# Performance work log

Measured on AMD Instinct MI355X. Metric: run time of the kernel, lower is better.

## Reference

```python
import jax, jax.numpy as jnp
import numpy as np

N_NODES = 100000
HEADS = 4
HEAD_DIM = 32  # hidden_channels // heads
NEG_SLOPE = 0.2


def gat_layer(x, W, a_src, a_dst, b, src, dst):
    # x: [N, Fin], W: [Fin, H*C], a_src/a_dst: [H, C], b: [H*C]
    N = x.shape[0]
    h = (x @ W).reshape(N, HEADS, HEAD_DIM)            # [N, H, C]
    alpha_s = jnp.einsum('nhc,hc->nh', h, a_src)       # [N, H]
    alpha_d = jnp.einsum('nhc,hc->nh', h, a_dst)       # [N, H]
    e = jax.nn.leaky_relu(alpha_s[src] + alpha_d[dst], NEG_SLOPE)  # [E, H]
    # segment softmax over edges grouped by destination node
    e_max = jax.ops.segment_max(e, dst, num_segments=N)           # [N, H]
    ex = jnp.exp(e - e_max[dst])                                   # [E, H]
    denom = jax.ops.segment_sum(ex, dst, num_segments=N)          # [N, H]
    alpha = ex / denom[dst]                                        # [E, H]
    msg = h[src] * alpha[:, :, None]                               # [E, H, C]
    out = jax.ops.segment_sum(msg, dst, num_segments=N)           # [N, H, C]
    return out.reshape(N, HEADS * HEAD_DIM) + b


def setup_inputs() -> dict:
    key = jax.random.key(0)
    ks = jax.random.split(key, 10)
    Fin, H, C = 128, HEADS, HEAD_DIM
    x = jax.random.normal(ks[0], (N_NODES, Fin), dtype=jnp.float32)
    edge_index = jax.random.randint(ks[1], (2, 1000000), 0, N_NODES, dtype=jnp.int64)
    s = 1.0 / np.sqrt(Fin)
    W1 = jax.random.normal(ks[2], (Fin, H * C), dtype=jnp.float32) * s
    a_src1 = jax.random.normal(ks[3], (H, C), dtype=jnp.float32) * 0.1
    a_dst1 = jax.random.normal(ks[4], (H, C), dtype=jnp.float32) * 0.1
    b1 = jnp.zeros((H * C,), dtype=jnp.float32)
    s2 = 1.0 / np.sqrt(H * C)
    W2 = jax.random.normal(ks[5], (H * C, H * C), dtype=jnp.float32) * s2
    a_src2 = jax.random.normal(ks[6], (H, C), dtype=jnp.float32) * 0.1
    a_dst2 = jax.random.normal(ks[7], (H, C), dtype=jnp.float32) * 0.1
    b2 = jnp.zeros((H * C,), dtype=jnp.float32)
    return {"x": x, "edge_index": edge_index, "W1": W1, "a_src1": a_src1,
            "a_dst1": a_dst1, "b1": b1, "W2": W2, "a_src2": a_src2,
            "a_dst2": a_dst2, "b2": b2}


def reference(x, edge_index, W1, a_src1, a_dst1, b1, W2, a_src2, a_dst2, b2):
    N = x.shape[0]
    # add self-loops (PyG add_self_loops=True)
    loop = jnp.arange(N, dtype=edge_index.dtype)
    src = jnp.concatenate([edge_index[0], loop])
    dst = jnp.concatenate([edge_index[1], loop])
    h = gat_layer(x, W1, a_src1, a_dst1, b1, src, dst)
    h = jax.nn.elu(h)
    h = gat_layer(h, W2, a_src2, a_dst2, b2, src, dst)
    h = jax.nn.elu(h)
    return h
```

## Files before the change

### kernel.cpp

```cpp
#include <hip/hip_runtime.h>
#include <math.h>

#define NHEADS 4
#define HDIM 32
#define F 128
#define ACH 16384

typedef __attribute__((ext_vector_type(8))) short bf16x8;
typedef __attribute__((ext_vector_type(4))) float f32x4;

__device__ __forceinline__ float lrelu(float v) { return v > 0.f ? v : 0.2f * v; }

__device__ __forceinline__ unsigned short cvt_bf16(float f) {
    unsigned u = __float_as_uint(f);
    u += 0x7fffu + ((u >> 16) & 1u);
    return (unsigned short)(u >> 16);
}

__global__ void k_packW(const float* __restrict__ W, const float* __restrict__ a_src,
                        const float* __restrict__ a_dst, short* __restrict__ Wb) {
    int idx = blockIdx.x * 256 + threadIdx.x;
    if (idx >= 36 * 512) return;
    int j    = idx & 7;
    int lane = (idx >> 3) & 63;
    int frag = idx >> 9;
    int kk = frag / 9, ct = frag % 9;
    int k = kk * 32 + (lane >> 4) * 8 + j;
    int col = lane & 15;
    float val;
    if (ct < 8) {
        val = W[k * F + ct * 16 + col];
    } else if (col < 8) {
        int head = col & 3;
        const float* av = (col < 4) ? a_src : a_dst;
        float sum = 0.f;
        #pragma unroll 8
        for (int c = 0; c < HDIM; ++c)
            sum += W[k * F + head * HDIM + c] * av[head * HDIM + c];
        val = sum;
    } else {
        val = 0.f;
    }
    Wb[idx] = (short)cvt_bf16(val);
}

template<bool ABF16>
__global__ __launch_bounds__(256) void k_gemm_mfma(
    const void* __restrict__ xv, const short* __restrict__ Wb,
    unsigned short* __restrict__ hbf, float* __restrict__ as_out,
    float* __restrict__ ad_out, int N)
{
    const int wid  = threadIdx.x >> 6;
    const int lane = threadIdx.x & 63;
    const int rowbase = blockIdx.x * 64 + wid * 16;
    const int row  = rowbase + (lane & 15);
    const int rowc = min(row, N - 1);
    const int col = lane & 15;

    f32x4 acc[9] = {};
    #pragma unroll
    for (int kk = 0; kk < 4; ++kk) {
        bf16x8 a;
        if constexpr (ABF16) {
            const unsigned short* xr =
                (const unsigned short*)xv + (size_t)rowc * F + (lane >> 4) * 8;
            a = *(const bf16x8*)(xr + kk * 32);
        } else {
            const float* xr = (const float*)xv + (size_t)rowc * F + (lane >> 4) * 8;
            float4 xa = *(const float4*)(xr + kk * 32);
            float4 xb = *(const float4*)(xr + kk * 32 + 4);
            a[0] = cvt_bf16(xa.x); a[1] = cvt_bf16(xa.y);
            a[2] = cvt_bf16(xa.z); a[3] = cvt_bf16(xa.w);
            a[4] = cvt_bf16(xb.x); a[5] = cvt_bf16(xb.y);
            a[6] = cvt_bf16(xb.z); a[7] = cvt_bf16(xb.w);
        }
        const bf16x8* bp = (const bf16x8*)(Wb + (size_t)(kk * 9) * 512 + lane * 8);
        #pragma unroll
        for (int ct = 0; ct < 9; ++ct) {
            bf16x8 b = bp[ct * 64];
            acc[ct] = __builtin_amdgcn_mfma_f32_16x16x32_bf16(a, b, acc[ct], 0, 0, 0);
        }
    }

    const int r0 = rowbase + (lane >> 4) * 4;
    #pragma unroll
    for (int i = 0; i < 4; ++i) {
        int r = r0 + i;
        if (r < N) {
            #pragma unroll
            for (int ct = 0; ct < 8; ++ct)
                hbf[(size_t)r * F + ct * 16 + col] = cvt_bf16(acc[ct][i]);
            if (col < 4)       as_out[r * NHEADS + col]     = acc[8][i];
            else if (col < 8)  ad_out[r * NHEADS + col - 4] = acc[8][i];
        }
    }
}


__global__ __launch_bounds__(256) void k_bhist(
    const int* __restrict__ src, const int* __restrict__ dst,
    int* __restrict__ bha, int nbuc, int E, int TOT)
{
    __shared__ int hist[512];
    int t = threadIdx.x;
    hist[t] = 0; hist[t + 256] = 0;
    __syncthreads();
    int base = blockIdx.x * ACH;
    #pragma unroll
    for (int k = 0; k < ACH / 256; ++k) {
        int i = base + k * 256 + t;
        if (i < TOT) {
            int d = (i < E) ? dst[i] : (i - E);
            atomicAdd(&hist[d >> 8], 1);
        }
    }
    __syncthreads();
    if (t < nbuc)        bha[(size_t)blockIdx.x * nbuc + t] = hist[t];
    if (t + 256 < nbuc)  bha[(size_t)blockIdx.x * nbuc + t + 256] = hist[t + 256];
}

__global__ __launch_bounds__(256) void k_bscan1(
    int* __restrict__ bha, int* __restrict__ btot, int nbuc, int nab)
{
    int t = blockIdx.x * 256 + threadIdx.x;
    if (t >= nbuc) return;
    int run = 0;
    int j = 0;
    for (; j + 4 <= nab; j += 4) {
        int v0 = bha[(size_t)(j + 0) * nbuc + t];
        int v1 = bha[(size_t)(j + 1) * nbuc + t];
        int v2 = bha[(size_t)(j + 2) * nbuc + t];
        int v3 = bha[(size_t)(j + 3) * nbuc + t];
        bha[(size_t)(j + 0) * nbuc + t] = run; run += v0;
        bha[(size_t)(j + 1) * nbuc + t] = run; run += v1;
        bha[(size_t)(j + 2) * nbuc + t] = run; run += v2;
        bha[(size_t)(j + 3) * nbuc + t] = run; run += v3;
    }
    for (; j < nab; ++j) {
        int v = bha[(size_t)j * nbuc + t];
        bha[(size_t)j * nbuc + t] = run; run += v;
    }
    btot[t] = run;
}

__global__ __launch_bounds__(512) void k_bscan2(
    const int* __restrict__ btot, int* __restrict__ bbase, int nbuc)
{
    __shared__ int sh[512];
    int t = threadIdx.x;
    int v = (t < nbuc) ? btot[t] : 0;
    sh[t] = v;
    __syncthreads();
    for (int off = 1; off < 512; off <<= 1) {
        int u = (t >= off) ? sh[t - off] : 0;
        __syncthreads();
        sh[t] += u;
        __syncthreads();
    }
    if (t < nbuc) {
        bbase[t] = sh[t] - v;
        if (t == nbuc - 1) bbase[nbuc] = sh[t];
    }
}

__global__ __launch_bounds__(256) void k_bscan3(
    int* __restrict__ bha, const int* __restrict__ bbase, int nbuc, int total)
{
    int i = blockIdx.x * 256 + threadIdx.x;
    if (i < total) bha[i] += bbase[i % nbuc];
}

__global__ __launch_bounds__(256) void k_bscatter(
    const int* __restrict__ src, const int* __restrict__ dst,
    const int* __restrict__ bha, int2* __restrict__ epairs,
    int nbuc, int E, int TOT)
{
    __shared__ int cur[512];
    int t = threadIdx.x;
    if (t < nbuc)       cur[t] = bha[(size_t)blockIdx.x * nbuc + t];
    if (t + 256 < nbuc) cur[t + 256] = bha[(size_t)blockIdx.x * nbuc + t + 256];
    __syncthreads();
    int base = blockIdx.x * ACH;
    #pragma unroll
    for (int k = 0; k < ACH / 256; ++k) {
        int i = base + k * 256 + t;
        if (i < TOT) {
            int s, d;
            if (i < E) { s = src[i]; d = dst[i]; } else { s = d = i - E; }
            int pos = atomicAdd(&cur[d >> 8], 1);
            epairs[pos] = make_int2(s, d);
        }
    }
}

__global__ __launch_bounds__(256) void k_bdeg(
    const int2* __restrict__ epairs, const int* __restrict__ bbase,
    int* __restrict__ deg, int N)
{
    __shared__ int hist[256];
    int t = threadIdx.x;
    hist[t] = 0;
    __syncthreads();
    int s0 = bbase[blockIdx.x], s1 = bbase[blockIdx.x + 1];
    for (int i = s0 + t; i < s1; i += 256)
        atomicAdd(&hist[epairs[i].y & 255], 1);
    __syncthreads();
    int node = blockIdx.x * 256 + t;
    if (node < N) deg[node] = hist[t];
}

__global__ __launch_bounds__(256) void k_nscatter(
    const int2* __restrict__ epairs, const int* __restrict__ bbase,
    const int* __restrict__ rowptr, int* __restrict__ ssrc, int N)
{
    __shared__ int cur[256];
    int t = threadIdx.x;
    int node = blockIdx.x * 256 + t;
    cur[t] = (node < N) ? rowptr[node] : 0;
    __syncthreads();
    int s0 = bbase[blockIdx.x], s1 = bbase[blockIdx.x + 1];
    for (int i = s0 + t; i < s1; i += 256) {
        int2 p = epairs[i];
        int pos = atomicAdd(&cur[p.y & 255], 1);
        ssrc[pos] = p.x;
    }
}

__global__ void k_scan1(const int* __restrict__ deg, int* __restrict__ tmp,
                        int* __restrict__ bsum, int N) {
    __shared__ int sh[256];
    int t = threadIdx.x, i = blockIdx.x * 256 + t;
    sh[t] = (i < N) ? deg[i] : 0;
    __syncthreads();
    for (int off = 1; off < 256; off <<= 1) {
        int u = (t >= off) ? sh[t - off] : 0;
        __syncthreads();
        sh[t] += u;
        __syncthreads();
    }
    if (i < N) tmp[i] = sh[t];
    if (t == 255) bsum[blockIdx.x] = sh[255];
}

__global__ void k_scan2(const int* __restrict__ bsum, int* __restrict__ ebsum, int nblk) {
    __shared__ int sh[512];
    int t = threadIdx.x;
    int v = (t < nblk) ? bsum[t] : 0;
    sh[t] = v;
    __syncthreads();
    for (int off = 1; off < 512; off <<= 1) {
        int u = (t >= off) ? sh[t - off] : 0;
        __syncthreads();
        sh[t] += u;
        __syncthreads();
    }
    if (t < nblk) ebsum[t] = sh[t] - v;
}

__global__ void k_scan3(const int* __restrict__ tmp, const int* __restrict__ ebsum,
                        const int* __restrict__ deg, int* __restrict__ rowptr, int N) {
    int i = blockIdx.x * 256 + threadIdx.x;
    if (i >= N) return;
    int incl = tmp[i] + ebsum[i >> 8];
    rowptr[i] = incl - deg[i];
    if (i == N - 1) rowptr[N] = incl;
}

__global__ __launch_bounds__(256) void k_sort_hist(
    const int* __restrict__ deg, int* __restrict__ bh, int N)
{
    __shared__ int hist[256];
    int t = threadIdx.x;
    hist[t] = 0;
    __syncthreads();
    int base = blockIdx.x * 1024;
    #pragma unroll
    for (int g = 0; g < 4; ++g) {
        int i = base + g * 256 + t;
        if (i < N) atomicAdd(&hist[min(deg[i], 255)], 1);
    }
    __syncthreads();
    bh[blockIdx.x * 256 + t] = hist[t];
}

__global__ __launch_bounds__(256) void k_sort_off(int* __restrict__ bh, int nb)
{
    int t = threadIdx.x;
    int run = 0;
    for (int j = 0; j < nb; ++j) {
        int v = bh[j * 256 + t];
        bh[j * 256 + t] = run;
        run += v;
    }
    __shared__ int sh[256];
    int tot = run;
    sh[t] = tot;
    __syncthreads();
    for (int off = 1; off < 256; off <<= 1) {
        int u = (t >= off) ? sh[t - off] : 0;
        __syncthreads();
        sh[t] += u;
        __syncthreads();
    }
    int bucket_base = sh[t] - tot;
    for (int j = 0; j < nb; ++j)
        bh[j * 256 + t] += bucket_base;
}

__global__ __launch_bounds__(256) void k_sort_scatter(
    const int* __restrict__ deg, const int* __restrict__ bh,
    int* __restrict__ order, int N)
{
    __shared__ int cur[256];
    int t = threadIdx.x;
    cur[t] = bh[blockIdx.x * 256 + t];
    __syncthreads();
    int base = blockIdx.x * 1024;
    #pragma unroll
    for (int g = 0; g < 4; ++g) {
        int i = base + g * 256 + t;
        if (i < N) {
            int pos = atomicAdd(&cur[min(deg[i], 255)], 1);
            order[pos] = i;
        }
    }
}

template<bool OUTBF16>
__global__ __launch_bounds__(256) void k_aggregate(
    const int* __restrict__ rowptr, const int* __restrict__ ssrc,
    const int* __restrict__ order,
    const float* __restrict__ as, const float* __restrict__ ad,
    const unsigned short* __restrict__ hbf, const float* __restrict__ bias,
    void* __restrict__ outv, int N)
{
    int gi = (blockIdx.x * 256 + threadIdx.x) >> 4;
    if (gi >= N) return;
    const int node  = order[gi];
    const int l16   = threadIdx.x & 15;
    const int hb    = l16 >> 2;
    const int c0    = l16 * 8;
    const int start = rowptr[node], end = rowptr[node + 1];
    const float adB = ad[node * NHEADS + hb];

    float a0=0.f,a1=0.f,a2=0.f,a3=0.f,a4=0.f,a5=0.f,a6=0.f,a7=0.f;
    float dacc = 0.f;
    for (int base = start; base < end; base += 8) {
        int   sj[8];
        float fj[8];
        uint4 hj[8];
        #pragma unroll
        for (int j = 0; j < 8; ++j)
            sj[j] = ssrc[min(base + j, end - 1)];
        #pragma unroll
        for (int j = 0; j < 8; ++j)
            fj[j] = as[sj[j] * NHEADS + hb];
        #pragma unroll
        for (int j = 0; j < 8; ++j)
            hj[j] = *(const uint4*)(hbf + (size_t)sj[j] * F + c0);
        #pragma unroll
        for (int j = 0; j < 8; ++j) {
            float ex = (base + j < end) ? __expf(lrelu(fj[j] + adB)) : 0.f;
            dacc += ex;
            a0 = fmaf(ex, __uint_as_float(hj[j].x << 16),         a0);
            a1 = fmaf(ex, __uint_as_float(hj[j].x & 0xffff0000u), a1);
            a2 = fmaf(ex, __uint_as_float(hj[j].y << 16),         a2);
            a3 = fmaf(ex, __uint_as_float(hj[j].y & 0xffff0000u), a3);
            a4 = fmaf(ex, __uint_as_float(hj[j].z << 16),         a4);
            a5 = fmaf(ex, __uint_as_float(hj[j].z & 0xffff0000u), a5);
            a6 = fmaf(ex, __uint_as_float(hj[j].w << 16),         a6);
            a7 = fmaf(ex, __uint_as_float(hj[j].w & 0xffff0000u), a7);
        }
    }
    float inv = 1.f / dacc;
    float v[8] = {a0,a1,a2,a3,a4,a5,a6,a7};
    #pragma unroll
    for (int k = 0; k < 8; ++k) {
        float t = v[k] * inv + bias[c0 + k];
        v[k] = t > 0.f ? t : expm1f(t);
    }
    if (OUTBF16) {
        unsigned r0 = (unsigned)cvt_bf16(v[0]) | ((unsigned)cvt_bf16(v[1]) << 16);
        unsigned r1 = (unsigned)cvt_bf16(v[2]) | ((unsigned)cvt_bf16(v[3]) << 16);
        unsigned r2 = (unsigned)cvt_bf16(v[4]) | ((unsigned)cvt_bf16(v[5]) << 16);
        unsigned r3 = (unsigned)cvt_bf16(v[6]) | ((unsigned)cvt_bf16(v[7]) << 16);
        uint4 o = {r0, r1, r2, r3};
        *(uint4*)((unsigned short*)outv + (size_t)node * F + c0) = o;
    } else {
        float4 o0 = {v[0], v[1], v[2], v[3]};
        float4 o1 = {v[4], v[5], v[6], v[7]};
        float* op = (float*)outv + (size_t)node * F + c0;
        *(float4*)op       = o0;
        *(float4*)(op + 4) = o1;
    }
}

extern "C" void kernel_launch(void* const* d_in, const int* in_sizes, int n_in,
                              void* d_out, int out_size, void* d_ws, size_t ws_size,
                              hipStream_t stream)
{
    const float* x      = (const float*)d_in[0];
    const int*   eidx   = (const int*)d_in[1];
    const float* W1     = (const float*)d_in[2];
    const float* a_src1 = (const float*)d_in[3];
    const float* a_dst1 = (const float*)d_in[4];
    const float* b1     = (const float*)d_in[5];
    const float* W2     = (const float*)d_in[6];
    const float* a_src2 = (const float*)d_in[7];
    const float* a_dst2 = (const float*)d_in[8];
    const float* b2     = (const float*)d_in[9];

    const int N = in_sizes[0] / F;
    const int E = in_sizes[1] / 2;
    const int TOT = E + N;
    const int* src = eidx;
    const int* dst = eidx + E;

    const int nbuc = (N + 255) / 256;
    const int nab  = (TOT + ACH - 1) / ACH;
    const int nblk = (N + 255) / 256;
    const int nb   = (N + 1023) / 1024;

    int2* epairs = (int2*)d_ws;
    unsigned short* hbf    = (unsigned short*)(epairs + TOT);
    unsigned short* out1bf = hbf + (size_t)N * F;
    float* as = (float*)(out1bf + (size_t)N * F);
    float* ad = as + (size_t)N * NHEADS;
    int* deg    = (int*)(ad + (size_t)N * NHEADS);
    int* rowptr = deg + N;
    int* bsum   = rowptr + N + 1;
    int* ebsum  = bsum + 512;
    int* tmp    = ebsum + 512;
    int* ssrc   = tmp + N;
    int* order  = ssrc + TOT;
    int* bh     = order + N;
    int* bha    = bh + (size_t)nb * 256;
    int* btot   = bha + (size_t)nab * nbuc;
    int* bbase  = btot + nbuc;
    short* Wb1  = (short*)(((uintptr_t)(bbase + nbuc + 1) + 15) & ~(uintptr_t)15);
    short* Wb2  = Wb1 + 36 * 512;

    const int gemmBlocks = (N + 63) / 64;
    const int aggBlocks  = (N + 15) / 16;

    k_packW<<<72, 256, 0, stream>>>(W1, a_src1, a_dst1, Wb1);
    k_packW<<<72, 256, 0, stream>>>(W2, a_src2, a_dst2, Wb2);

    k_bhist<<<nab, 256, 0, stream>>>(src, dst, bha, nbuc, E, TOT);
    k_bscan1<<<(nbuc + 255) / 256, 256, 0, stream>>>(bha, btot, nbuc, nab);
    k_bscan2<<<1, 512, 0, stream>>>(btot, bbase, nbuc);
    k_bscan3<<<(nab * nbuc + 255) / 256, 256, 0, stream>>>(bha, bbase, nbuc, nab * nbuc);
    k_bscatter<<<nab, 256, 0, stream>>>(src, dst, bha, epairs, nbuc, E, TOT);
    k_bdeg<<<nbuc, 256, 0, stream>>>(epairs, bbase, deg, N);
    k_scan1<<<nblk, 256, 0, stream>>>(deg, tmp, bsum, N);
    k_scan2<<<1, 512, 0, stream>>>(bsum, ebsum, nblk);
    k_scan3<<<nblk, 256, 0, stream>>>(tmp, ebsum, deg, rowptr, N);
    k_nscatter<<<nbuc, 256, 0, stream>>>(epairs, bbase, rowptr, ssrc, N);

    k_sort_hist<<<nb, 256, 0, stream>>>(deg, bh, N);
    k_sort_off<<<1, 256, 0, stream>>>(bh, nb);
    k_sort_scatter<<<nb, 256, 0, stream>>>(deg, bh, order, N);

    k_gemm_mfma<false><<<gemmBlocks, 256, 0, stream>>>(x, Wb1, hbf, as, ad, N);
    k_aggregate<true><<<aggBlocks, 256, 0, stream>>>(rowptr, ssrc, order, as, ad, hbf, b1, out1bf, N);

    k_gemm_mfma<true><<<gemmBlocks, 256, 0, stream>>>(out1bf, Wb2, hbf, as, ad, N);
    k_aggregate<false><<<aggBlocks, 256, 0, stream>>>(rowptr, ssrc, order, as, ad, hbf, b2, d_out, N);
}
```

Before: 291.4 us.

## Fuse per-bucket degree, scan and scatter into one kernel; widen aggregate batch

Bucket-local degree counts, the row-pointer prefix scan and the node scatter now run in one kernel per 256-node bucket. Each bucket's base offset is already known from the bucket scan, so the global three-pass scan over node degrees is dropped, which removes four kernel launches and their intermediate buffers. Separately, the aggregation loop now gathers 16 neighbours per iteration instead of 8 to put more loads in flight. The wider batch raises register pressure and wastes more clamped loads on low-degree nodes.

```diff
diff --git a/kernel.cpp b/kernel.cpp
--- a/kernel.cpp
+++ b/kernel.cpp
@@ -193,11 +193,14 @@
     }
 }
 
-__global__ __launch_bounds__(256) void k_bdeg(
+__global__ __launch_bounds__(256) void k_bfinal(
     const int2* __restrict__ epairs, const int* __restrict__ bbase,
-    int* __restrict__ deg, int N)
+    int* __restrict__ deg, int* __restrict__ rowptr, int* __restrict__ ssrc,
+    int N, int nbuc)
 {
     __shared__ int hist[256];
+    __shared__ int sh[256];
+    __shared__ int cur[256];
     int t = threadIdx.x;
     hist[t] = 0;
     __syncthreads();
@@ -205,65 +208,29 @@
     for (int i = s0 + t; i < s1; i += 256)
         atomicAdd(&hist[epairs[i].y & 255], 1);
     __syncthreads();
+    int h = hist[t];
+    sh[t] = h;
+    __syncthreads();
+    for (int off = 1; off < 256; off <<= 1) {
+        int u = (t >= off) ? sh[t - off] : 0;
+        __syncthreads();
+        sh[t] += u;
+        __syncthreads();
+    }
     int node = blockIdx.x * 256 + t;
-    if (node < N) deg[node] = hist[t];
-}
-
-__global__ __launch_bounds__(256) void k_nscatter(
-    const int2* __restrict__ epairs, const int* __restrict__ bbase,
-    const int* __restrict__ rowptr, int* __restrict__ ssrc, int N)
-{
-    __shared__ int cur[256];
-    int t = threadIdx.x;
-    int node = blockIdx.x * 256 + t;
-    cur[t] = (node < N) ? rowptr[node] : 0;
-    __syncthreads();
-    int s0 = bbase[blockIdx.x], s1 = bbase[blockIdx.x + 1];
+    int excl = s0 + sh[t] - h;
+    cur[t] = excl;
+    if (node < N) {
+        deg[node] = h;
+        rowptr[node] = excl;
+    }
+    if (node == 0) rowptr[N] = bbase[nbuc];
+    __syncthreads();
     for (int i = s0 + t; i < s1; i += 256) {
         int2 p = epairs[i];
         int pos = atomicAdd(&cur[p.y & 255], 1);
         ssrc[pos] = p.x;
     }
-}
-
-__global__ void k_scan1(const int* __restrict__ deg, int* __restrict__ tmp,
-                        int* __restrict__ bsum, int N) {
-    __shared__ int sh[256];
-    int t = threadIdx.x, i = blockIdx.x * 256 + t;
-    sh[t] = (i < N) ? deg[i] : 0;
-    __syncthreads();
-    for (int off = 1; off < 256; off <<= 1) {
-        int u = (t >= off) ? sh[t - off] : 0;
-        __syncthreads();
-        sh[t] += u;
-        __syncthreads();
-    }
-    if (i < N) tmp[i] = sh[t];
-    if (t == 255) bsum[blockIdx.x] = sh[255];
-}
-
-__global__ void k_scan2(const int* __restrict__ bsum, int* __restrict__ ebsum, int nblk) {
-    __shared__ int sh[512];
-    int t = threadIdx.x;
-    int v = (t < nblk) ? bsum[t] : 0;
-    sh[t] = v;
-    __syncthreads();
-    for (int off = 1; off < 512; off <<= 1) {
-        int u = (t >= off) ? sh[t - off] : 0;
-        __syncthreads();
-        sh[t] += u;
-        __syncthreads();
-    }
-    if (t < nblk) ebsum[t] = sh[t] - v;
-}
-
-__global__ void k_scan3(const int* __restrict__ tmp, const int* __restrict__ ebsum,
-                        const int* __restrict__ deg, int* __restrict__ rowptr, int N) {
-    int i = blockIdx.x * 256 + threadIdx.x;
-    if (i >= N) return;
-    int incl = tmp[i] + ebsum[i >> 8];
-    rowptr[i] = incl - deg[i];
-    if (i == N - 1) rowptr[N] = incl;
 }
 
 __global__ __launch_bounds__(256) void k_sort_hist(
@@ -345,21 +312,21 @@
 
     float a0=0.f,a1=0.f,a2=0.f,a3=0.f,a4=0.f,a5=0.f,a6=0.f,a7=0.f;
     float dacc = 0.f;
-    for (int base = start; base < end; base += 8) {
-        int   sj[8];
-        float fj[8];
-        uint4 hj[8];
+    for (int base = start; base < end; base += 16) {
+        int   sj[16];
+        float fj[16];
+        uint4 hj[16];
         #pragma unroll
-        for (int j = 0; j < 8; ++j)
+        for (int j = 0; j < 16; ++j)
             sj[j] = ssrc[min(base + j, end - 1)];
         #pragma unroll
-        for (int j = 0; j < 8; ++j)
+        for (int j = 0; j < 16; ++j)
             fj[j] = as[sj[j] * NHEADS + hb];
         #pragma unroll
-        for (int j = 0; j < 8; ++j)
+        for (int j = 0; j < 16; ++j)
             hj[j] = *(const uint4*)(hbf + (size_t)sj[j] * F + c0);
         #pragma unroll
-        for (int j = 0; j < 8; ++j) {
+        for (int j = 0; j < 16; ++j) {
             float ex = (base + j < end) ? __expf(lrelu(fj[j] + adB)) : 0.f;
             dacc += ex;
             a0 = fmaf(ex, __uint_as_float(hj[j].x << 16),         a0);
@@ -418,7 +385,6 @@
 
     const int nbuc = (N + 255) / 256;
     const int nab  = (TOT + ACH - 1) / ACH;
-    const int nblk = (N + 255) / 256;
     const int nb   = (N + 1023) / 1024;
 
     int2* epairs = (int2*)d_ws;
@@ -428,10 +394,7 @@
     float* ad = as + (size_t)N * NHEADS;
     int* deg    = (int*)(ad + (size_t)N * NHEADS);
     int* rowptr = deg + N;
-    int* bsum   = rowptr + N + 1;
-    int* ebsum  = bsum + 512;
-    int* tmp    = ebsum + 512;
-    int* ssrc   = tmp + N;
+    int* ssrc   = rowptr + N + 1;
     int* order  = ssrc + TOT;
     int* bh     = order + N;
     int* bha    = bh + (size_t)nb * 256;
@@ -451,11 +414,7 @@
     k_bscan2<<<1, 512, 0, stream>>>(btot, bbase, nbuc);
     k_bscan3<<<(nab * nbuc + 255) / 256, 256, 0, stream>>>(bha, bbase, nbuc, nab * nbuc);
     k_bscatter<<<nab, 256, 0, stream>>>(src, dst, bha, epairs, nbuc, E, TOT);
-    k_bdeg<<<nbuc, 256, 0, stream>>>(epairs, bbase, deg, N);
-    k_scan1<<<nblk, 256, 0, stream>>>(deg, tmp, bsum, N);
-    k_scan2<<<1, 512, 0, stream>>>(bsum, ebsum, nblk);
-    k_scan3<<<nblk, 256, 0, stream>>>(tmp, ebsum, deg, rowptr, N);
-    k_nscatter<<<nbuc, 256, 0, stream>>>(epairs, bbase, rowptr, ssrc, N);
+    k_bfinal<<<nbuc, 256, 0, stream>>>(epairs, bbase, deg, rowptr, ssrc, N, nbuc);
 
     k_sort_hist<<<nb, 256, 0, stream>>>(deg, bh, N);
     k_sort_off<<<1, 256, 0, stream>>>(bh, nb);
```

Result: no change. 294.4 us (+1.0%).
